# Kernel optimization log

Hardware: AMD Instinct MI355X
Metric: run time of the kernel (lower is better)

## Reference

```python
import jax, jax.numpy as jnp
import numpy as np

NEG = -9e15
N_NODES, IN_DIM, H1, H2, HEADS, DEC, N_EDGES, B_PAIRS = 4096, 512, 256, 128, 4, 512, 131072, 4096


def setup_inputs() -> dict:
    key = jax.random.key(0)
    ks = jax.random.split(key, 24)
    d = {}
    d["x_o"] = jax.random.normal(ks[0], (N_NODES, IN_DIM), jnp.float32)
    d["x_a"] = jax.random.normal(ks[1], (N_NODES, IN_DIM), jnp.float32)
    d["edge_index"] = jax.random.randint(ks[2], (2, N_EDGES), 0, N_NODES)
    d["idx"] = jax.random.randint(ks[3], (2, B_PAIRS), 0, N_NODES)
    # GAT layer 1 (in=IN_DIM, out=H1), per-head stacked params
    d["W1"] = jax.random.normal(ks[4], (HEADS, IN_DIM, H1)) * (IN_DIM ** -0.5)
    d["a1"] = jax.random.normal(ks[5], (HEADS, 2 * H1)) * 0.1
    d["lin1"] = jax.random.normal(ks[6], (HEADS * H1, H1)) * ((HEADS * H1) ** -0.5)
    d["res1"] = jax.random.normal(ks[7], (IN_DIM, H1)) * (IN_DIM ** -0.5)
    # GAT layer 2 (in=H1, out=H2)
    d["W2"] = jax.random.normal(ks[8], (HEADS, H1, H2)) * (H1 ** -0.5)
    d["a2"] = jax.random.normal(ks[9], (HEADS, 2 * H2)) * 0.1
    d["lin2"] = jax.random.normal(ks[10], (HEADS * H2, H2)) * ((HEADS * H2) ** -0.5)
    d["res2"] = jax.random.normal(ks[11], (H1, H2)) * (H1 ** -0.5)
    # heads
    d["mlp1_w"] = jax.random.normal(ks[12], (H2, H2)) * (H2 ** -0.5)
    d["mlp1_b"] = jnp.zeros((H2,))
    d["disc_w"] = jax.random.normal(ks[13], (H2, H2)) * (H2 ** -0.5)
    d["disc_b"] = jnp.zeros(())
    d["dec1_w"] = jax.random.normal(ks[14], (2 * H2, DEC)) * ((2 * H2) ** -0.5)
    d["dec1_b"] = jnp.zeros((DEC,))
    d["dec2_w"] = jax.random.normal(ks[15], (DEC, 1)) * (DEC ** -0.5)
    d["dec2_b"] = jnp.zeros((1,))
    d["adv_w"] = jax.random.normal(ks[16], (H2, H2)) * (H2 ** -0.5)
    d["adv_b"] = jnp.zeros((H2,))
    return d


def _gat_residual_layer(h, mask, W, a, lin, res):
    # W: [H, Fin, Fo], a: [H, 2*Fo]. e_ij = leakyrelu(Wh_i . a[:Fo] + Wh_j . a[Fo:])
    # (algebraically identical to the NxN all-pairs concat @ a in the torch code).
    def head(Wk, ak):
        Wh = h @ Wk                      # [N, Fo]
        Fo = Wk.shape[1]
        src = Wh @ ak[:Fo]               # [N]
        dst = Wh @ ak[Fo:]               # [N]
        e = jax.nn.leaky_relu(src[:, None] + dst[None, :], 0.2)  # [N, N]
        att = jax.nn.softmax(jnp.where(mask, e, NEG), axis=1)
        return jax.nn.elu(att @ Wh)      # [N, Fo]

    heads = jax.vmap(head)(W, a)         # [H, N, Fo]
    Hn, N, Fo = heads.shape
    concat = jnp.transpose(heads, (1, 0, 2)).reshape(N, Hn * Fo)
    mh = jax.nn.elu(concat @ lin)
    return jax.nn.relu(mh + h @ res)     # relu(relu(x)) == relu(x); dropout off in eval


def reference(x_o, x_a, W1, a1, lin1, res1, W2, a2, lin2, res2,
              mlp1_w, mlp1_b, disc_w, disc_b, dec1_w, dec1_b,
              dec2_w, dec2_b, adv_w, adv_b, edge_index, idx):
    N = x_o.shape[0]
    mask = jnp.zeros((N, N), jnp.bool_).at[edge_index[0], edge_index[1]].set(True)

    def encode(x):
        h = _gat_residual_layer(x, mask, W1, a1, lin1, res1)
        h = _gat_residual_layer(h, mask, W2, a2, lin2, res2)
        return h

    x2_o = encode(x_o)                   # [N, H2]
    x2_o_a = encode(x_a)

    h_os = jax.nn.sigmoid(x2_o.mean(0)) @ mlp1_w + mlp1_b      # [H2]
    h_os_a = jax.nn.sigmoid(x2_o_a.mean(0)) @ mlp1_w + mlp1_b

    def disc(c, h_pl, h_mi):  # Bilinear(h, c) with out=1
        sc1 = (h_pl @ disc_w) @ c + disc_b
        sc2 = (h_mi @ disc_w) @ c + disc_b
        return jnp.stack([sc1, sc2], axis=1)                    # [N, 2]

    ret_os = disc(h_os, x2_o, x2_o_a)
    ret_os_a = disc(h_os_a, x2_o_a, x2_o)

    # extract_entities, default branch (task_type not in {LDA, MDA, LMI})
    entity1 = x2_o[idx[0]]
    entity2 = x2_o[idx[1]]
    z = jnp.concatenate([entity1, entity2], axis=1)             # [B, 2*H2]
    hdec = jax.nn.relu(z @ dec1_w + dec1_b)
    log1 = hdec @ dec2_w + dec2_b                               # [B, 1]
    log = jax.nn.sigmoid(log1)

    sc_1 = (x2_o @ adv_w + adv_b).sum(1)[None, :]               # [1, N]
    sc_2 = (x2_o_a @ adv_w + adv_b).sum(1)[None, :]
    logits = jnp.concatenate([sc_1, sc_2], axis=1)              # [1, 2N]

    return (log, ret_os, ret_os_a, x2_o, logits, log1)
```

## Files before the change

kernel.cpp:

```cpp
#include <hip/hip_runtime.h>
#include <stdint.h>

#define N_NODES 4096
#define N_EDGES 131072

typedef __attribute__((ext_vector_type(8))) short short8;
typedef __attribute__((ext_vector_type(4))) float floatx4;

__device__ __forceinline__ float bf2f(unsigned short u) {
  union { unsigned u; float f; } v; v.u = ((unsigned)u) << 16; return v.f;
}
__device__ __forceinline__ unsigned short f2bf(float f) {
  union { float f; unsigned u; } v; v.f = f;
  unsigned r = 0x7FFFu + ((v.u >> 16) & 1u);
  return (unsigned short)((v.u + r) >> 16);
}
__device__ __forceinline__ float wredsum(float x) {
#pragma unroll
  for (int d = 32; d >= 1; d >>= 1) x += __shfl_xor(x, d);
  return x;
}
__device__ __forceinline__ float wredmax(float x) {
#pragma unroll
  for (int d = 32; d >= 1; d >>= 1) x = fmaxf(x, __shfl_xor(x, d));
  return x;
}
__device__ __forceinline__ void gload16(const void* g, void* l) {
  __builtin_amdgcn_global_load_lds(
      (const __attribute__((address_space(1))) unsigned*)g,
      (__attribute__((address_space(3))) unsigned*)l, 16, 0, 0);
}

__global__ __launch_bounds__(256) void gemm128(
    const unsigned short* __restrict__ A, const unsigned short* __restrict__ Bt,
    int M, int N, int K, unsigned short* __restrict__ Cb) {
  __shared__ __align__(16) unsigned short As[128 * 32];
  __shared__ __align__(16) unsigned short Bs[128 * 32];
  const int t = threadIdx.x, lane = t & 63, w = t >> 6;
  const int wr = w >> 1, wc = w & 1;
  const int n0 = blockIdx.x * 128, m0 = blockIdx.y * 128;
  floatx4 acc[4][4] = {};
  const int arow = t >> 2;
  const int schunk = (t & 3) ^ ((arow >> 1) & 3);

  for (int kt = 0; kt < K; kt += 32) {
    __syncthreads();
    gload16(A + (size_t)(m0 + arow) * K + kt + schunk * 8, &As[t * 8]);
    gload16(A + (size_t)(m0 + 64 + arow) * K + kt + schunk * 8, &As[(256 + t) * 8]);
    gload16(Bt + (size_t)(n0 + arow) * K + kt + schunk * 8, &Bs[t * 8]);
    gload16(Bt + (size_t)(n0 + 64 + arow) * K + kt + schunk * 8, &Bs[(256 + t) * 8]);
    __syncthreads();
    short8 af[4], bfr[4];
    const int koff = lane >> 4;
#pragma unroll
    for (int m = 0; m < 4; ++m) {
      const int r = wr * 64 + (lane & 15) + m * 16;
      af[m] = *(const short8*)&As[r * 32 + ((koff ^ ((r >> 1) & 3)) << 3)];
    }
#pragma unroll
    for (int n = 0; n < 4; ++n) {
      const int r = wc * 64 + (lane & 15) + n * 16;
      bfr[n] = *(const short8*)&Bs[r * 32 + ((koff ^ ((r >> 1) & 3)) << 3)];
    }
#pragma unroll
    for (int m = 0; m < 4; ++m)
#pragma unroll
      for (int n = 0; n < 4; ++n)
        acc[m][n] = __builtin_amdgcn_mfma_f32_16x16x32_bf16(af[m], bfr[n], acc[m][n], 0, 0, 0);
  }

  const int rb = m0 + wr * 64 + (lane >> 4) * 4;
  const int cb = n0 + wc * 64 + (lane & 15);
#pragma unroll
  for (int m = 0; m < 4; ++m)
#pragma unroll
    for (int n = 0; n < 4; ++n) {
      const int col = cb + n * 16;
#pragma unroll
      for (int r = 0; r < 4; ++r) {
        const int row = rb + m * 16 + r;
        Cb[(size_t)row * N + col] = f2bf(acc[m][n][r]);
      }
    }
}

__device__ __forceinline__ void stage64(const unsigned short* __restrict__ G,
                                        unsigned short* lds, int row0, int K,
                                        int kt, int t) {
  const int l0 = t, l1 = t + 256;
  const int r0 = l0 >> 3, c0 = l0 & 7;
  const int r1 = l1 >> 3, c1 = l1 & 7;
  gload16(G + (size_t)(row0 + r0) * K + kt + ((c0 ^ (r0 & 7)) << 3), &lds[l0 * 8]);
  gload16(G + (size_t)(row0 + r1) * K + kt + ((c1 ^ (r1 & 7)) << 3), &lds[l1 * 8]);
}
__device__ __forceinline__ short8 frag64(const unsigned short* lds, int r, int c) {
  return *(const short8*)&lds[r * 64 + ((c ^ (r & 7)) << 3)];
}

template <int EP>
__global__ __launch_bounds__(256) void gemm64(
    const unsigned short* __restrict__ A, const unsigned short* __restrict__ Bt,
    int M, int N, int K, unsigned short* __restrict__ Cb,
    const float* __restrict__ bias) {
  __shared__ __align__(16) unsigned short As[64 * 64];
  __shared__ __align__(16) unsigned short Bs[64 * 64];
  const int t = threadIdx.x, lane = t & 63, w = t >> 6;
  const int wr = w >> 1, wc = w & 1;
  const int n0 = blockIdx.x * 64, m0 = blockIdx.y * 64;
  floatx4 acc[2][2] = {};

  for (int kt = 0; kt < K; kt += 64) {
    __syncthreads();
    stage64(A, As, m0, K, kt, t);
    stage64(Bt, Bs, n0, K, kt, t);
    __syncthreads();
    short8 af[2][2], bfv[2][2];
#pragma unroll
    for (int m = 0; m < 2; ++m) {
      const int ra = wr * 32 + (lane & 15) + m * 16;
#pragma unroll
      for (int kk = 0; kk < 2; ++kk)
        af[m][kk] = frag64(As, ra, (lane >> 4) + kk * 4);
    }
#pragma unroll
    for (int n = 0; n < 2; ++n) {
      const int rb = wc * 32 + (lane & 15) + n * 16;
#pragma unroll
      for (int kk = 0; kk < 2; ++kk)
        bfv[n][kk] = frag64(Bs, rb, (lane >> 4) + kk * 4);
    }
#pragma unroll
    for (int kk = 0; kk < 2; ++kk)
#pragma unroll
      for (int m = 0; m < 2; ++m)
#pragma unroll
        for (int n = 0; n < 2; ++n)
          acc[m][n] = __builtin_amdgcn_mfma_f32_16x16x32_bf16(af[m][kk], bfv[n][kk], acc[m][n], 0, 0, 0);
  }

  const int rb = m0 + wr * 32 + (lane >> 4) * 4;
  const int cb = n0 + wc * 32 + (lane & 15);
#pragma unroll
  for (int m = 0; m < 2; ++m)
#pragma unroll
    for (int n = 0; n < 2; ++n) {
      const int col = cb + n * 16;
#pragma unroll
      for (int r = 0; r < 4; ++r) {
        const int row = rb + m * 16 + r;
        float v = acc[m][n][r];
        if (EP == 4) { v += bias[col]; v = v > 0.f ? v : 0.f; }
        Cb[(size_t)row * N + col] = f2bf(v);
      }
    }
}

template <int EP>
__global__ __launch_bounds__(256) void gemm64dual(
    const unsigned short* __restrict__ A1, const unsigned short* __restrict__ B1t, int K1,
    const unsigned short* __restrict__ A2, const unsigned short* __restrict__ B2t, int K2,
    int N, unsigned short* __restrict__ Cb,
    float* __restrict__ Cfo, float* __restrict__ Cfa) {
  __shared__ __align__(16) unsigned short As[64 * 64];
  __shared__ __align__(16) unsigned short Bs[64 * 64];
  const int t = threadIdx.x, lane = t & 63, w = t >> 6;
  const int wr = w >> 1, wc = w & 1;
  const int n0 = blockIdx.x * 64, m0 = blockIdx.y * 64;
  floatx4 acc[2][2] = {};

#pragma unroll 1
  for (int pass = 0; pass < 2; ++pass) {
    const unsigned short* A = pass ? A2 : A1;
    const unsigned short* Bt = pass ? B2t : B1t;
    const int K = pass ? K2 : K1;
    for (int kt = 0; kt < K; kt += 64) {
      __syncthreads();
      stage64(A, As, m0, K, kt, t);
      stage64(Bt, Bs, n0, K, kt, t);
      __syncthreads();
      short8 af[2][2], bfv[2][2];
#pragma unroll
      for (int m = 0; m < 2; ++m) {
        const int ra = wr * 32 + (lane & 15) + m * 16;
#pragma unroll
        for (int kk = 0; kk < 2; ++kk)
          af[m][kk] = frag64(As, ra, (lane >> 4) + kk * 4);
      }
#pragma unroll
      for (int n = 0; n < 2; ++n) {
        const int rb = wc * 32 + (lane & 15) + n * 16;
#pragma unroll
        for (int kk = 0; kk < 2; ++kk)
          bfv[n][kk] = frag64(Bs, rb, (lane >> 4) + kk * 4);
      }
#pragma unroll
      for (int kk = 0; kk < 2; ++kk)
#pragma unroll
        for (int m = 0; m < 2; ++m)
#pragma unroll
          for (int n = 0; n < 2; ++n)
            acc[m][n] = __builtin_amdgcn_mfma_f32_16x16x32_bf16(af[m][kk], bfv[n][kk], acc[m][n], 0, 0, 0);
    }
    if (pass == 0) {
#pragma unroll
      for (int m = 0; m < 2; ++m)
#pragma unroll
        for (int n = 0; n < 2; ++n)
#pragma unroll
          for (int r = 0; r < 4; ++r) {
            float v = acc[m][n][r];
            acc[m][n][r] = v > 0.f ? v : expm1f(v);
          }
    }
  }

  const int rb = m0 + wr * 32 + (lane >> 4) * 4;
  const int cb = n0 + wc * 32 + (lane & 15);
#pragma unroll
  for (int m = 0; m < 2; ++m)
#pragma unroll
    for (int n = 0; n < 2; ++n) {
      const int col = cb + n * 16;
#pragma unroll
      for (int r = 0; r < 4; ++r) {
        const int row = rb + m * 16 + r;
        float v = acc[m][n][r];
        v = v > 0.f ? v : 0.f;
        if (EP == 0) {
          Cb[(size_t)row * N + col] = f2bf(v);
        } else {
          float* bb = (row < 4096) ? Cfo : Cfa;
          bb[(size_t)(row & 4095) * N + col] = v;
        }
      }
    }
}

__global__ __launch_bounds__(256) void scatter_kernel(
    const int* __restrict__ ei, unsigned long long* __restrict__ mb) {
  int e = blockIdx.x * 256 + threadIdx.x;
  if (e < N_EDGES) {
    int r = ei[e], c = ei[N_EDGES + e];
    atomicOr(&mb[(size_t)r * 64 + (c >> 6)], 1ull << (c & 63));
  }
}

__global__ __launch_bounds__(256) void pack2_kernel(
    const float* W1, const float* lin1, const float* res1, const float* W2,
    const float* lin2, const float* res2, const float* dec1,
    const float* xo, const float* xa,
    unsigned short* dW1, unsigned short* dlin1, unsigned short* dres1,
    unsigned short* dW2, unsigned short* dlin2, unsigned short* dres2,
    unsigned short* ddec1, unsigned short* x16) {
  const int b = blockIdx.x, t = threadIdx.x;
  if (b >= 1248) {
    int ib = b - 1248;
    const float* src = (ib < 512) ? xo : xa;
    unsigned short* dst = x16 + ((ib < 512) ? 0 : (size_t)4096 * 512);
    size_t base = (size_t)(ib & 511) * 4096;
#pragma unroll
    for (int q = 0; q < 4; ++q) {
      size_t o = base + q * 1024 + t * 4;
      float4 v = *(const float4*)&src[o];
      ushort4 u = {f2bf(v.x), f2bf(v.y), f2bf(v.z), f2bf(v.w)};
      *(ushort4*)&dst[o] = u;
    }
    return;
  }
  const float* src; unsigned short* dst; int K, F, nFt, tb;
  if (b < 512)       { int h = b >> 7;        src = W1 + h * 131072; dst = dW1 + h * 131072; K = 512;  F = 256; nFt = 8;  tb = b & 127; }
  else if (b < 768)  {                        src = lin1;            dst = dlin1;            K = 1024; F = 256; nFt = 8;  tb = b - 512; }
  else if (b < 896)  {                        src = res1;            dst = dres1;            K = 512;  F = 256; nFt = 8;  tb = b - 768; }
  else if (b < 1024) { int h = (b - 896) >> 5; src = W2 + h * 32768; dst = dW2 + h * 32768;  K = 256;  F = 128; nFt = 4;  tb = (b - 896) & 31; }
  else if (b < 1088) {                        src = lin2;            dst = dlin2;            K = 512;  F = 128; nFt = 4;  tb = b - 1024; }
  else if (b < 1120) {                        src = res2;            dst = dres2;            K = 256;  F = 128; nFt = 4;  tb = b - 1088; }
  else               {                        src = dec1;            dst = ddec1;            K = 256;  F = 512; nFt = 16; tb = b - 1120; }
  const int k0 = (tb / nFt) * 32, f0 = (tb % nFt) * 32;
  __shared__ float tile[32][33];
  {
    int r = t >> 3, c4 = (t & 7) * 4;
    float4 v = *(const float4*)&src[(size_t)(k0 + r) * F + f0 + c4];
    tile[r][c4] = v.x; tile[r][c4 + 1] = v.y; tile[r][c4 + 2] = v.z; tile[r][c4 + 3] = v.w;
  }
  __syncthreads();
  {
    int f = t >> 3, k4 = (t & 7) * 4;
    ushort4 u;
    u.x = f2bf(tile[k4 + 0][f]); u.y = f2bf(tile[k4 + 1][f]);
    u.z = f2bf(tile[k4 + 2][f]); u.w = f2bf(tile[k4 + 3][f]);
    *(ushort4*)&dst[(size_t)(f0 + f) * K + k0 + k4] = u;
  }
}

__global__ __launch_bounds__(256) void srcdst_kernel(
    const unsigned short* __restrict__ Wh, const float* __restrict__ a,
    float* __restrict__ sd, int FO) {
  int lane = threadIdx.x & 63, wv = threadIdx.x >> 6;
  int i = blockIdx.x * 4 + wv;
  int W = 4 * FO;
  for (int h = 0; h < 4; ++h) {
    float s = 0.f, d = 0.f;
    for (int f = lane; f < FO; f += 64) {
      float wh = bf2f(Wh[(size_t)i * W + h * FO + f]);
      s += wh * a[h * 2 * FO + f];
      d += wh * a[h * 2 * FO + FO + f];
    }
    s = wredsum(s);
    d = wredsum(d);
    if (lane == 0) { sd[i * 8 + h] = s; sd[i * 8 + 4 + h] = d; }
  }
}

template <int FO>
__global__ __launch_bounds__(256) void attn_kernel(
    const unsigned long long* __restrict__ mb, const float* __restrict__ sd,
    const unsigned short* __restrict__ Wh, unsigned short* __restrict__ outp) {
  constexpr int E = FO / 64;
  constexpr int W = 4 * FO;
  constexpr int WGCAP = 512;
  __shared__ unsigned short nbr[4104];
  __shared__ float wgs[4][WGCAP + 8];
  __shared__ int s_cnt;
  const int i = blockIdx.x;
  const int mrow = i & 4095;
  const int base = i & ~4095;
  const int t = threadIdx.x;
  const int lane = t & 63, h = t >> 6;

  if (t < 64) {
    unsigned long long wb = mb[(size_t)mrow * 64 + t];
    int pc = __popcll(wb);
    int inc = pc;
#pragma unroll
    for (int d = 1; d < 64; d <<= 1) {
      int v = __shfl_up(inc, d);
      if (t >= d) inc += v;
    }
    if (t == 63) s_cnt = inc;
    int off = inc - pc;
    while (wb) {
      int b = __builtin_ctzll(wb);
      nbr[off++] = (unsigned short)(t * 64 + b);
      wb &= wb - 1;
    }
  }
  __syncthreads();
  const int cnt = s_cnt;
  if (t < 8) nbr[(cnt + t < 4103) ? cnt + t : 4103] = 0;
  const float src_i = sd[(size_t)i * 8 + h];
  float acc[E] = {};
  float inv = 1.f;
  if (cnt > 0) {
    float m = -1e30f;
    for (int nn = lane; nn < cnt; nn += 64) {
      int j = base + nbr[nn];
      float x = src_i + sd[(size_t)j * 8 + 4 + h];
      m = fmaxf(m, x > 0.f ? x : 0.2f * x);
    }
    m = wredmax(m);
    float ssum = 0.f;
    for (int nn = lane; nn < cnt; nn += 64) {
      int j = base + nbr[nn];
      float x = src_i + sd[(size_t)j * 8 + 4 + h];
      float e = x > 0.f ? x : 0.2f * x;
      float g = __expf(e - m);
      if (nn < WGCAP) wgs[h][nn] = g;
      ssum += g;
    }
    ssum = wredsum(ssum);
    inv = 1.f / ssum;
    if (lane < 8) wgs[h][((cnt < WGCAP ? cnt : WGCAP) + lane)] = 0.f;
    __builtin_amdgcn_s_barrier();
    const int lim = cnt < WGCAP ? cnt : WGCAP;
    const int limr = (lim + 7) & ~7;
    for (int nn = 0; nn < limr; nn += 8) {
      ushort4 ja = *(const ushort4*)&nbr[nn];
      ushort4 jb = *(const ushort4*)&nbr[nn + 4];
      float4 wa = *(const float4*)&wgs[h][nn];
      float4 wb4 = *(const float4*)&wgs[h][nn + 4];
      const int js[8] = {ja.x, ja.y, ja.z, ja.w, jb.x, jb.y, jb.z, jb.w};
      const float ws[8] = {wa.x, wa.y, wa.z, wa.w, wb4.x, wb4.y, wb4.z, wb4.w};
      if constexpr (E == 4) {
        uint2 r[8];
#pragma unroll
        for (int q = 0; q < 8; ++q)
          r[q] = *(const uint2*)(Wh + (size_t)(base + js[q]) * W + h * FO + lane * E);
#pragma unroll
        for (int q = 0; q < 8; ++q) {
          acc[0] += ws[q] * bf2f((unsigned short)(r[q].x & 0xffff));
          acc[1] += ws[q] * bf2f((unsigned short)(r[q].x >> 16));
          acc[2] += ws[q] * bf2f((unsigned short)(r[q].y & 0xffff));
          acc[3] += ws[q] * bf2f((unsigned short)(r[q].y >> 16));
        }
      } else {
        unsigned r[8];
#pragma unroll
        for (int q = 0; q < 8; ++q)
          r[q] = *(const unsigned*)(Wh + (size_t)(base + js[q]) * W + h * FO + lane * E);
#pragma unroll
        for (int q = 0; q < 8; ++q) {
          acc[0] += ws[q] * bf2f((unsigned short)(r[q] & 0xffff));
          acc[1] += ws[q] * bf2f((unsigned short)(r[q] >> 16));
        }
      }
    }
    for (int nn = WGCAP; nn < cnt; ++nn) {
      int j = base + nbr[nn];
      float x = src_i + sd[(size_t)j * 8 + 4 + h];
      float e = x > 0.f ? x : 0.2f * x;
      float g = __expf(e - m);
      const unsigned short* p = Wh + (size_t)j * W + h * FO + lane * E;
#pragma unroll
      for (int q = 0; q < E; ++q) acc[q] += g * bf2f(p[q]);
    }
  } else {
    const float wg = 1.f / 4096.f;
    for (int j = 0; j < N_NODES; ++j) {
      const unsigned short* p = Wh + (size_t)(base + j) * W + h * FO + lane * E;
#pragma unroll
      for (int q = 0; q < E; ++q) acc[q] += wg * bf2f(p[q]);
    }
  }
  unsigned short* op = outp + (size_t)i * W + h * FO + lane * E;
#pragma unroll
  for (int q = 0; q < E; ++q) {
    float v = acc[q] * inv;
    op[q] = f2bf(v > 0.f ? v : expm1f(v));
  }
}

__global__ __launch_bounds__(128) void colsum_kernel(
    const float* __restrict__ x2o, const float* __restrict__ x2a,
    float* __restrict__ small) {
  int b = blockIdx.x, f = threadIdx.x;
  const float* x = (b < 64) ? x2o : x2a;
  float* s = (b < 64) ? small : (small + 128);
  int r0 = (b & 63) * 64;
  float acc = 0.f;
  for (int r = 0; r < 64; ++r) acc += x[(size_t)(r0 + r) * 128 + f];
  atomicAdd(&s[f], acc);
}

__global__ __launch_bounds__(128) void finalize_kernel(
    float* __restrict__ small, const float* __restrict__ mlp1_w,
    const float* __restrict__ mlp1_b, const float* __restrict__ disc_w,
    const float* __restrict__ adv_w, const float* __restrict__ adv_b) {
  __shared__ float so[128], sa[128], ho[128], ha[128];
  int f = threadIdx.x;
  so[f] = 1.f / (1.f + __expf(-small[f] * (1.f / 4096.f)));
  sa[f] = 1.f / (1.f + __expf(-small[128 + f] * (1.f / 4096.f)));
  __syncthreads();
  float aco = mlp1_b[f], aca = mlp1_b[f];
  for (int c = 0; c < 128; ++c) {
    aco += so[c] * mlp1_w[c * 128 + f];
    aca += sa[c] * mlp1_w[c * 128 + f];
  }
  ho[f] = aco;
  ha[f] = aca;
  __syncthreads();
  float vo = 0.f, va = 0.f, ar = 0.f;
  for (int c = 0; c < 128; ++c) {
    vo += disc_w[f * 128 + c] * ho[c];
    va += disc_w[f * 128 + c] * ha[c];
    ar += adv_w[f * 128 + c];
  }
  small[256 + f] = vo;
  small[384 + f] = va;
  small[512 + f] = ar;
  if (f == 0) {
    float b = 0.f;
    for (int c = 0; c < 128; ++c) b += adv_b[c];
    small[640] = b;
  }
}

__global__ __launch_bounds__(256) void pernode_kernel(
    const float* __restrict__ x2o, const float* __restrict__ x2a,
    const float* __restrict__ small, const float* __restrict__ disc_b,
    float* __restrict__ out) {
  const float* v_os = small + 256;
  const float* v_a = small + 384;
  const float* adv_rs = small + 512;
  int lane = threadIdx.x & 63, wv = threadIdx.x >> 6;
  int i = blockIdx.x * 4 + wv;
  float2 xo = *(const float2*)&x2o[(size_t)i * 128 + lane * 2];
  float2 xa = *(const float2*)&x2a[(size_t)i * 128 + lane * 2];
  float2 vo = *(const float2*)&v_os[lane * 2];
  float2 va = *(const float2*)&v_a[lane * 2];
  float2 ar = *(const float2*)&adv_rs[lane * 2];
  float poo = wredsum(xo.x * vo.x + xo.y * vo.y);
  float pao = wredsum(xa.x * vo.x + xa.y * vo.y);
  float paa = wredsum(xa.x * va.x + xa.y * va.y);
  float poa = wredsum(xo.x * va.x + xo.y * va.y);
  float pov = wredsum(xo.x * ar.x + xo.y * ar.y);
  float pav = wredsum(xa.x * ar.x + xa.y * ar.y);
  if (lane == 0) {
    float db = disc_b[0], bv = small[640];
    out[4096 + 2 * i] = poo + db;
    out[4096 + 2 * i + 1] = pao + db;
    out[12288 + 2 * i] = paa + db;
    out[12288 + 2 * i + 1] = poa + db;
    out[544768 + i] = pov + bv;
    out[548864 + i] = pav + bv;
  }
}

__global__ __launch_bounds__(256) void gather_kernel(
    const float* __restrict__ x2o, const int* __restrict__ idx,
    unsigned short* __restrict__ z) {
  int i = blockIdx.x, c = threadIdx.x;
  int s = (c < 128) ? idx[i] : idx[4096 + i];
  z[(size_t)i * 256 + c] = f2bf(x2o[(size_t)s * 128 + (c & 127)]);
}

__global__ __launch_bounds__(256) void dec2_kernel(
    const unsigned short* __restrict__ hdec, const float* __restrict__ w2,
    const float* __restrict__ b2, float* __restrict__ out) {
  int lane = threadIdx.x & 63, wv = threadIdx.x >> 6;
  int i = blockIdx.x * 4 + wv;
  float s = 0.f;
#pragma unroll
  for (int q = 0; q < 8; ++q) {
    int f = lane + q * 64;
    s += bf2f(hdec[(size_t)i * 512 + f]) * w2[f];
  }
  s = wredsum(s);
  if (lane == 0) {
    float v = s + b2[0];
    out[552960 + i] = v;
    out[i] = 1.f / (1.f + __expf(-v));
  }
}

extern "C" void kernel_launch(void* const* d_in, const int* in_sizes, int n_in,
                              void* d_out, int out_size, void* d_ws, size_t ws_size,
                              hipStream_t stream) {
  const float* x_o = (const float*)d_in[0];
  const float* x_a = (const float*)d_in[1];
  const int* ei = (const int*)d_in[2];
  const int* idx = (const int*)d_in[3];
  const float* W1 = (const float*)d_in[4];
  const float* a1 = (const float*)d_in[5];
  const float* lin1 = (const float*)d_in[6];
  const float* res1 = (const float*)d_in[7];
  const float* W2 = (const float*)d_in[8];
  const float* a2 = (const float*)d_in[9];
  const float* lin2 = (const float*)d_in[10];
  const float* res2 = (const float*)d_in[11];
  const float* mlp1_w = (const float*)d_in[12];
  const float* mlp1_b = (const float*)d_in[13];
  const float* disc_w = (const float*)d_in[14];
  const float* disc_b = (const float*)d_in[15];
  const float* dec1_w = (const float*)d_in[16];
  const float* dec1_b = (const float*)d_in[17];
  const float* dec2_w = (const float*)d_in[18];
  const float* dec2_b = (const float*)d_in[19];
  const float* adv_w = (const float*)d_in[20];
  const float* adv_b = (const float*)d_in[21];
  float* out = (float*)d_out;

  char* w = (char*)d_ws;
  size_t off = 0;
  auto alloc = [&](size_t b) {
    char* p = w + off;
    off += (b + 255) & ~(size_t)255;
    return p;
  };
  unsigned long long* mb = (unsigned long long*)alloc((size_t)4096 * 64 * 8);
  unsigned short* x16 = (unsigned short*)alloc((size_t)8192 * 512 * 2);
  unsigned short* Wh1 = (unsigned short*)alloc((size_t)8192 * 1024 * 2);
  unsigned short* ho1 = (unsigned short*)alloc((size_t)8192 * 1024 * 2);
  unsigned short* h1 = (unsigned short*)alloc((size_t)8192 * 256 * 2);
  unsigned short* Wh2 = (unsigned short*)alloc((size_t)8192 * 512 * 2);
  unsigned short* ho2 = (unsigned short*)alloc((size_t)8192 * 512 * 2);
  float* x2a = (float*)alloc((size_t)4096 * 128 * 4);
  float* sd1 = (float*)alloc((size_t)8192 * 8 * 4);
  float* sd2 = (float*)alloc((size_t)8192 * 8 * 4);
  float* small = (float*)alloc(1024 * 4);
  unsigned short* tW1 = (unsigned short*)alloc((size_t)524288 * 2);
  unsigned short* tlin1 = (unsigned short*)alloc((size_t)262144 * 2);
  unsigned short* tres1 = (unsigned short*)alloc((size_t)131072 * 2);
  unsigned short* tW2 = (unsigned short*)alloc((size_t)131072 * 2);
  unsigned short* tlin2 = (unsigned short*)alloc((size_t)65536 * 2);
  unsigned short* tres2 = (unsigned short*)alloc((size_t)32768 * 2);
  unsigned short* tdec1 = (unsigned short*)alloc((size_t)131072 * 2);
  unsigned short* z16 = (unsigned short*)alloc((size_t)4096 * 256 * 2);
  unsigned short* hdec = (unsigned short*)alloc((size_t)4096 * 512 * 2);

  hipMemsetAsync(mb, 0, (size_t)4096 * 64 * 8, stream);
  hipMemsetAsync(small, 0, 1024, stream);
  scatter_kernel<<<512, 256, 0, stream>>>(ei, mb);
  pack2_kernel<<<2272, 256, 0, stream>>>(W1, lin1, res1, W2, lin2, res2, dec1_w,
                                         x_o, x_a, tW1, tlin1, tres1, tW2,
                                         tlin2, tres2, tdec1, x16);

  float* x2o_out = out + 20480;

  gemm128<<<dim3(8, 64), 256, 0, stream>>>(x16, tW1, 8192, 1024, 512, Wh1);
  srcdst_kernel<<<2048, 256, 0, stream>>>(Wh1, a1, sd1, 256);
  attn_kernel<256><<<8192, 256, 0, stream>>>(mb, sd1, Wh1, ho1);
  gemm64dual<0><<<dim3(4, 128), 256, 0, stream>>>(ho1, tlin1, 1024, x16, tres1, 512, 256, h1, nullptr, nullptr);
  gemm128<<<dim3(4, 64), 256, 0, stream>>>(h1, tW2, 8192, 512, 256, Wh2);
  srcdst_kernel<<<2048, 256, 0, stream>>>(Wh2, a2, sd2, 128);
  attn_kernel<128><<<8192, 256, 0, stream>>>(mb, sd2, Wh2, ho2);
  gemm64dual<1><<<dim3(2, 128), 256, 0, stream>>>(ho2, tlin2, 512, h1, tres2, 256, 128, nullptr, x2o_out, x2a);

  colsum_kernel<<<128, 128, 0, stream>>>(x2o_out, x2a, small);
  finalize_kernel<<<1, 128, 0, stream>>>(small, mlp1_w, mlp1_b, disc_w, adv_w, adv_b);
  pernode_kernel<<<1024, 256, 0, stream>>>(x2o_out, x2a, small, disc_b, out);
  gather_kernel<<<4096, 256, 0, stream>>>(x2o_out, idx, z16);
  gemm64<4><<<dim3(8, 64), 256, 0, stream>>>(z16, tdec1, 4096, 512, 256, hdec, dec1_b);
  dec2_kernel<<<1024, 256, 0, stream>>>(hdec, dec2_w, dec2_b, out);
}
```

Baseline: 215.5 us.

## Fuse src/dst attention scores into GEMM epilogue and split neighbors across waves

Removes the separate srcdst kernels. The per-node attention projections are now computed in the gemm128 epilogue, reduced with shuffles and accumulated with atomics into sd buffers that the scatter kernel zeros. The attention kernel now splits the neighbor list across all four waves, each wave covering every head, and sums the partial results through LDS. Nodes with no neighbors take an early-exit path. The aim is fewer launches and better load balance and locality in neighbor aggregation. The cost is extra atomics, more registers for the per-head accumulators, and an extra LDS reduction.

```diff
diff --git a/kernel.cpp b/kernel.cpp
--- a/kernel.cpp
+++ b/kernel.cpp
@@ -33,7 +33,8 @@
 
 __global__ __launch_bounds__(256) void gemm128(
     const unsigned short* __restrict__ A, const unsigned short* __restrict__ Bt,
-    int M, int N, int K, unsigned short* __restrict__ Cb) {
+    int M, int N, int K, unsigned short* __restrict__ Cb,
+    const float* __restrict__ avec, float* __restrict__ sdv, int FO) {
   __shared__ __align__(16) unsigned short As[128 * 32];
   __shared__ __align__(16) unsigned short Bs[128 * 32];
   const int t = threadIdx.x, lane = t & 63, w = t >> 6;
@@ -82,6 +83,38 @@
         Cb[(size_t)row * N + col] = f2bf(acc[m][n][r]);
       }
     }
+
+  if (avec) {
+    const int h = n0 / FO;
+    const int cw0 = cb - h * FO;
+    float as_[4], ad_[4];
+#pragma unroll
+    for (int n = 0; n < 4; ++n) {
+      as_[n] = avec[h * 2 * FO + cw0 + n * 16];
+      ad_[n] = avec[h * 2 * FO + FO + cw0 + n * 16];
+    }
+#pragma unroll
+    for (int m = 0; m < 4; ++m)
+#pragma unroll
+      for (int r = 0; r < 4; ++r) {
+        float sp = 0.f, dp = 0.f;
+#pragma unroll
+        for (int n = 0; n < 4; ++n) {
+          sp += acc[m][n][r] * as_[n];
+          dp += acc[m][n][r] * ad_[n];
+        }
+#pragma unroll
+        for (int d = 1; d < 16; d <<= 1) {
+          sp += __shfl_xor(sp, d);
+          dp += __shfl_xor(dp, d);
+        }
+        if ((lane & 15) == 0) {
+          const int row = rb + m * 16 + r;
+          atomicAdd(&sdv[row * 8 + h], sp);
+          atomicAdd(&sdv[row * 8 + 4 + h], dp);
+        }
+      }
+  }
 }
 
 __device__ __forceinline__ void stage64(const unsigned short* __restrict__ G,
@@ -237,11 +270,17 @@
 }
 
 __global__ __launch_bounds__(256) void scatter_kernel(
-    const int* __restrict__ ei, unsigned long long* __restrict__ mb) {
-  int e = blockIdx.x * 256 + threadIdx.x;
-  if (e < N_EDGES) {
+    const int* __restrict__ ei, unsigned long long* __restrict__ mb,
+    float* __restrict__ sd1, float* __restrict__ sd2) {
+  int b = blockIdx.x;
+  if (b < 512) {
+    int e = b * 256 + threadIdx.x;
     int r = ei[e], c = ei[N_EDGES + e];
     atomicOr(&mb[(size_t)r * 64 + (c >> 6)], 1ull << (c & 63));
+  } else {
+    int z = (b - 512) * 256 + threadIdx.x;
+    if (z < 65536) sd1[z] = 0.f;
+    else sd2[z - 65536] = 0.f;
   }
 }
 
@@ -292,25 +331,6 @@
   }
 }
 
-__global__ __launch_bounds__(256) void srcdst_kernel(
-    const unsigned short* __restrict__ Wh, const float* __restrict__ a,
-    float* __restrict__ sd, int FO) {
-  int lane = threadIdx.x & 63, wv = threadIdx.x >> 6;
-  int i = blockIdx.x * 4 + wv;
-  int W = 4 * FO;
-  for (int h = 0; h < 4; ++h) {
-    float s = 0.f, d = 0.f;
-    for (int f = lane; f < FO; f += 64) {
-      float wh = bf2f(Wh[(size_t)i * W + h * FO + f]);
-      s += wh * a[h * 2 * FO + f];
-      d += wh * a[h * 2 * FO + FO + f];
-    }
-    s = wredsum(s);
-    d = wredsum(d);
-    if (lane == 0) { sd[i * 8 + h] = s; sd[i * 8 + 4 + h] = d; }
-  }
-}
-
 template <int FO>
 __global__ __launch_bounds__(256) void attn_kernel(
     const unsigned long long* __restrict__ mb, const float* __restrict__ sd,
@@ -318,14 +338,17 @@
   constexpr int E = FO / 64;
   constexpr int W = 4 * FO;
   constexpr int WGCAP = 512;
-  __shared__ unsigned short nbr[4104];
-  __shared__ float wgs[4][WGCAP + 8];
+  __shared__ __align__(16) char smem[8208 + 8320];
+  unsigned short* nbr = (unsigned short*)smem;
+  float (*wgs)[520] = (float (*)[520])(smem + 8208);
+  float* red = (float*)smem;
   __shared__ int s_cnt;
+  __shared__ float s_inv[4];
   const int i = blockIdx.x;
   const int mrow = i & 4095;
   const int base = i & ~4095;
   const int t = threadIdx.x;
-  const int lane = t & 63, h = t >> 6;
+  const int lane = t & 63, wv = t >> 6;
 
   if (t < 64) {
     unsigned long long wb = mb[(size_t)mrow * 64 + t];
@@ -346,39 +369,59 @@
   }
   __syncthreads();
   const int cnt = s_cnt;
+
+  if (cnt == 0) {
+    const float wg = 1.f / 4096.f;
+    float acc0[E] = {};
+    for (int j = 0; j < N_NODES; ++j) {
+      const unsigned short* p = Wh + (size_t)(base + j) * W + wv * FO + lane * E;
+#pragma unroll
+      for (int q = 0; q < E; ++q) acc0[q] += wg * bf2f(p[q]);
+    }
+    unsigned short* op = outp + (size_t)i * W + wv * FO + lane * E;
+#pragma unroll
+    for (int q = 0; q < E; ++q) {
+      float v = acc0[q];
+      op[q] = f2bf(v > 0.f ? v : expm1f(v));
+    }
+    return;
+  }
+
   if (t < 8) nbr[(cnt + t < 4103) ? cnt + t : 4103] = 0;
-  const float src_i = sd[(size_t)i * 8 + h];
-  float acc[E] = {};
-  float inv = 1.f;
-  if (cnt > 0) {
-    float m = -1e30f;
-    for (int nn = lane; nn < cnt; nn += 64) {
-      int j = base + nbr[nn];
-      float x = src_i + sd[(size_t)j * 8 + 4 + h];
-      m = fmaxf(m, x > 0.f ? x : 0.2f * x);
-    }
-    m = wredmax(m);
-    float ssum = 0.f;
-    for (int nn = lane; nn < cnt; nn += 64) {
-      int j = base + nbr[nn];
-      float x = src_i + sd[(size_t)j * 8 + 4 + h];
-      float e = x > 0.f ? x : 0.2f * x;
-      float g = __expf(e - m);
-      if (nn < WGCAP) wgs[h][nn] = g;
-      ssum += g;
-    }
-    ssum = wredsum(ssum);
-    inv = 1.f / ssum;
-    if (lane < 8) wgs[h][((cnt < WGCAP ? cnt : WGCAP) + lane)] = 0.f;
-    __builtin_amdgcn_s_barrier();
-    const int lim = cnt < WGCAP ? cnt : WGCAP;
-    const int limr = (lim + 7) & ~7;
-    for (int nn = 0; nn < limr; nn += 8) {
-      ushort4 ja = *(const ushort4*)&nbr[nn];
-      ushort4 jb = *(const ushort4*)&nbr[nn + 4];
+  const float src_i = sd[(size_t)i * 8 + wv];
+  float m = -1e30f;
+  for (int nn = lane; nn < cnt; nn += 64) {
+    int j = base + nbr[nn];
+    float x = src_i + sd[(size_t)j * 8 + 4 + wv];
+    m = fmaxf(m, x > 0.f ? x : 0.2f * x);
+  }
+  m = wredmax(m);
+  float ssum = 0.f;
+  for (int nn = lane; nn < cnt; nn += 64) {
+    int j = base + nbr[nn];
+    float x = src_i + sd[(size_t)j * 8 + 4 + wv];
+    float e = x > 0.f ? x : 0.2f * x;
+    float g = __expf(e - m);
+    if (nn < WGCAP) wgs[wv][nn] = g;
+    ssum += g;
+  }
+  ssum = wredsum(ssum);
+  if (lane == 0) s_inv[wv] = 1.f / ssum;
+  if (lane < 8) wgs[wv][(cnt < WGCAP ? cnt : WGCAP) + lane] = 0.f;
+  __syncthreads();
+
+  float acc[4][E] = {};
+  const int lim = cnt < WGCAP ? cnt : WGCAP;
+  const int ngroups = (lim + 7) >> 3;
+  for (int g = wv; g < ngroups; g += 4) {
+    const int nn = g * 8;
+    ushort4 ja = *(const ushort4*)&nbr[nn];
+    ushort4 jb = *(const ushort4*)&nbr[nn + 4];
+    const int js[8] = {ja.x, ja.y, ja.z, ja.w, jb.x, jb.y, jb.z, jb.w};
+#pragma unroll
+    for (int h = 0; h < 4; ++h) {
       float4 wa = *(const float4*)&wgs[h][nn];
       float4 wb4 = *(const float4*)&wgs[h][nn + 4];
-      const int js[8] = {ja.x, ja.y, ja.z, ja.w, jb.x, jb.y, jb.z, jb.w};
       const float ws[8] = {wa.x, wa.y, wa.z, wa.w, wb4.x, wb4.y, wb4.z, wb4.w};
       if constexpr (E == 4) {
         uint2 r[8];
@@ -387,10 +430,10 @@
           r[q] = *(const uint2*)(Wh + (size_t)(base + js[q]) * W + h * FO + lane * E);
 #pragma unroll
         for (int q = 0; q < 8; ++q) {
-          acc[0] += ws[q] * bf2f((unsigned short)(r[q].x & 0xffff));
-          acc[1] += ws[q] * bf2f((unsigned short)(r[q].x >> 16));
-          acc[2] += ws[q] * bf2f((unsigned short)(r[q].y & 0xffff));
-          acc[3] += ws[q] * bf2f((unsigned short)(r[q].y >> 16));
+          acc[h][0] += ws[q] * bf2f((unsigned short)(r[q].x & 0xffff));
+          acc[h][1] += ws[q] * bf2f((unsigned short)(r[q].x >> 16));
+          acc[h][2] += ws[q] * bf2f((unsigned short)(r[q].y & 0xffff));
+          acc[h][3] += ws[q] * bf2f((unsigned short)(r[q].y >> 16));
         }
       } else {
         unsigned r[8];
@@ -399,32 +442,39 @@
           r[q] = *(const unsigned*)(Wh + (size_t)(base + js[q]) * W + h * FO + lane * E);
 #pragma unroll
         for (int q = 0; q < 8; ++q) {
-          acc[0] += ws[q] * bf2f((unsigned short)(r[q] & 0xffff));
-          acc[1] += ws[q] * bf2f((unsigned short)(r[q] >> 16));
+          acc[h][0] += ws[q] * bf2f((unsigned short)(r[q] & 0xffff));
+          acc[h][1] += ws[q] * bf2f((unsigned short)(r[q] >> 16));
         }
       }
     }
-    for (int nn = WGCAP; nn < cnt; ++nn) {
-      int j = base + nbr[nn];
-      float x = src_i + sd[(size_t)j * 8 + 4 + h];
-      float e = x > 0.f ? x : 0.2f * x;
-      float g = __expf(e - m);
-      const unsigned short* p = Wh + (size_t)j * W + h * FO + lane * E;
-#pragma unroll
-      for (int q = 0; q < E; ++q) acc[q] += g * bf2f(p[q]);
-    }
-  } else {
-    const float wg = 1.f / 4096.f;
-    for (int j = 0; j < N_NODES; ++j) {
-      const unsigned short* p = Wh + (size_t)(base + j) * W + h * FO + lane * E;
-#pragma unroll
-      for (int q = 0; q < E; ++q) acc[q] += wg * bf2f(p[q]);
-    }
-  }
-  unsigned short* op = outp + (size_t)i * W + h * FO + lane * E;
+  }
+  for (int nn = WGCAP; nn < cnt; ++nn) {
+    int j = base + nbr[nn];
+    float x = src_i + sd[(size_t)j * 8 + 4 + wv];
+    float e = x > 0.f ? x : 0.2f * x;
+    float g = __expf(e - m);
+    const unsigned short* p = Wh + (size_t)j * W + wv * FO + lane * E;
+#pragma unroll
+    for (int q = 0; q < E; ++q) acc[wv][q] += g * bf2f(p[q]);
+  }
+  __syncthreads();
+#pragma unroll
+  for (int h = 0; h < 4; ++h)
+#pragma unroll
+    for (int q = 0; q < E; ++q)
+      red[(wv * 4 + h) * 64 * E + lane * E + q] = acc[h][q];
+  __syncthreads();
+  float fin[E] = {};
+#pragma unroll
+  for (int w2 = 0; w2 < 4; ++w2)
+#pragma unroll
+    for (int q = 0; q < E; ++q)
+      fin[q] += red[(w2 * 4 + wv) * 64 * E + lane * E + q];
+  const float inv = s_inv[wv];
+  unsigned short* op = outp + (size_t)i * W + wv * FO + lane * E;
 #pragma unroll
   for (int q = 0; q < E; ++q) {
-    float v = acc[q] * inv;
+    float v = fin[q] * inv;
     op[q] = f2bf(v > 0.f ? v : expm1f(v));
   }
 }
@@ -589,19 +639,17 @@
 
   hipMemsetAsync(mb, 0, (size_t)4096 * 64 * 8, stream);
   hipMemsetAsync(small, 0, 1024, stream);
-  scatter_kernel<<<512, 256, 0, stream>>>(ei, mb);
+  scatter_kernel<<<1024, 256, 0, stream>>>(ei, mb, sd1, sd2);
   pack2_kernel<<<2272, 256, 0, stream>>>(W1, lin1, res1, W2, lin2, res2, dec1_w,
                                          x_o, x_a, tW1, tlin1, tres1, tW2,
                                          tlin2, tres2, tdec1, x16);
 
   float* x2o_out = out + 20480;
 
-  gemm128<<<dim3(8, 64), 256, 0, stream>>>(x16, tW1, 8192, 1024, 512, Wh1);
-  srcdst_kernel<<<2048, 256, 0, stream>>>(Wh1, a1, sd1, 256);
+  gemm128<<<dim3(8, 64), 256, 0, stream>>>(x16, tW1, 8192, 1024, 512, Wh1, a1, sd1, 256);
   attn_kernel<256><<<8192, 256, 0, stream>>>(mb, sd1, Wh1, ho1);
   gemm64dual<0><<<dim3(4, 128), 256, 0, stream>>>(ho1, tlin1, 1024, x16, tres1, 512, 256, h1, nullptr, nullptr);
-  gemm128<<<dim3(4, 64), 256, 0, stream>>>(h1, tW2, 8192, 512, 256, Wh2);
-  srcdst_kernel<<<2048, 256, 0, stream>>>(Wh2, a2, sd2, 128);
+  gemm128<<<dim3(4, 64), 256, 0, stream>>>(h1, tW2, 8192, 512, 256, Wh2, a2, sd2, 128);
   attn_kernel<128><<<8192, 256, 0, stream>>>(mb, sd2, Wh2, ho2);
   gemm64dual<1><<<dim3(2, 128), 256, 0, stream>>>(ho2, tlin2, 512, h1, tres2, 256, 128, nullptr, x2o_out, x2a);
 
```

After: 232.6 us. +7.9%, slower.

## Fuse attention src/dst projections into GEMM epilogue and double-buffer neighbor gathers

Applied to the files above, without the earlier changes.

The per-node src/dst attention scores are now computed in the gemm128 epilogue from the fp32 accumulators, using shuffle reductions and atomicAdd into sd buffers. The scatter kernel zeroes those buffers first. This removes two srcdst kernel launches and the re-read of Wh from memory. Separately, the attention kernel's neighbor aggregation loop is software-pipelined with two register buffers of 8 gathered rows, so loads for the next group are in flight during the FMAs of the current one. The padding of the shared arrays is enlarged to cover the prefetch overrun. The costs are float atomics, whose ordering is nondeterministic and shifts scores slightly because they come from unrounded accumulators, plus higher register pressure in attn.

```diff
diff --git a/kernel.cpp b/kernel.cpp
--- a/kernel.cpp
+++ b/kernel.cpp
@@ -33,7 +33,8 @@
 
 __global__ __launch_bounds__(256) void gemm128(
     const unsigned short* __restrict__ A, const unsigned short* __restrict__ Bt,
-    int M, int N, int K, unsigned short* __restrict__ Cb) {
+    int M, int N, int K, unsigned short* __restrict__ Cb,
+    const float* __restrict__ avec, float* __restrict__ sdv, int FO) {
   __shared__ __align__(16) unsigned short As[128 * 32];
   __shared__ __align__(16) unsigned short Bs[128 * 32];
   const int t = threadIdx.x, lane = t & 63, w = t >> 6;
@@ -82,6 +83,38 @@
         Cb[(size_t)row * N + col] = f2bf(acc[m][n][r]);
       }
     }
+
+  if (avec) {
+    const int h = n0 / FO;
+    const int cw0 = cb - h * FO;
+    float as_[4], ad_[4];
+#pragma unroll
+    for (int n = 0; n < 4; ++n) {
+      as_[n] = avec[h * 2 * FO + cw0 + n * 16];
+      ad_[n] = avec[h * 2 * FO + FO + cw0 + n * 16];
+    }
+#pragma unroll
+    for (int m = 0; m < 4; ++m)
+#pragma unroll
+      for (int r = 0; r < 4; ++r) {
+        float sp = 0.f, dp = 0.f;
+#pragma unroll
+        for (int n = 0; n < 4; ++n) {
+          sp += acc[m][n][r] * as_[n];
+          dp += acc[m][n][r] * ad_[n];
+        }
+#pragma unroll
+        for (int d = 1; d < 16; d <<= 1) {
+          sp += __shfl_xor(sp, d);
+          dp += __shfl_xor(dp, d);
+        }
+        if ((lane & 15) == 0) {
+          const int row = rb + m * 16 + r;
+          atomicAdd(&sdv[row * 8 + h], sp);
+          atomicAdd(&sdv[row * 8 + 4 + h], dp);
+        }
+      }
+  }
 }
 
 __device__ __forceinline__ void stage64(const unsigned short* __restrict__ G,
@@ -237,11 +270,17 @@
 }
 
 __global__ __launch_bounds__(256) void scatter_kernel(
-    const int* __restrict__ ei, unsigned long long* __restrict__ mb) {
-  int e = blockIdx.x * 256 + threadIdx.x;
-  if (e < N_EDGES) {
+    const int* __restrict__ ei, unsigned long long* __restrict__ mb,
+    float* __restrict__ sd1, float* __restrict__ sd2) {
+  int b = blockIdx.x;
+  if (b < 512) {
+    int e = b * 256 + threadIdx.x;
     int r = ei[e], c = ei[N_EDGES + e];
     atomicOr(&mb[(size_t)r * 64 + (c >> 6)], 1ull << (c & 63));
+  } else {
+    int z = (b - 512) * 256 + threadIdx.x;
+    if (z < 65536) sd1[z] = 0.f;
+    else sd2[z - 65536] = 0.f;
   }
 }
 
@@ -292,25 +331,6 @@
   }
 }
 
-__global__ __launch_bounds__(256) void srcdst_kernel(
-    const unsigned short* __restrict__ Wh, const float* __restrict__ a,
-    float* __restrict__ sd, int FO) {
-  int lane = threadIdx.x & 63, wv = threadIdx.x >> 6;
-  int i = blockIdx.x * 4 + wv;
-  int W = 4 * FO;
-  for (int h = 0; h < 4; ++h) {
-    float s = 0.f, d = 0.f;
-    for (int f = lane; f < FO; f += 64) {
-      float wh = bf2f(Wh[(size_t)i * W + h * FO + f]);
-      s += wh * a[h * 2 * FO + f];
-      d += wh * a[h * 2 * FO + FO + f];
-    }
-    s = wredsum(s);
-    d = wredsum(d);
-    if (lane == 0) { sd[i * 8 + h] = s; sd[i * 8 + 4 + h] = d; }
-  }
-}
-
 template <int FO>
 __global__ __launch_bounds__(256) void attn_kernel(
     const unsigned long long* __restrict__ mb, const float* __restrict__ sd,
@@ -318,8 +338,8 @@
   constexpr int E = FO / 64;
   constexpr int W = 4 * FO;
   constexpr int WGCAP = 512;
-  __shared__ unsigned short nbr[4104];
-  __shared__ float wgs[4][WGCAP + 8];
+  __shared__ unsigned short nbr[4136];
+  __shared__ float wgs[4][WGCAP + 32];
   __shared__ int s_cnt;
   const int i = blockIdx.x;
   const int mrow = i & 4095;
@@ -346,7 +366,7 @@
   }
   __syncthreads();
   const int cnt = s_cnt;
-  if (t < 8) nbr[(cnt + t < 4103) ? cnt + t : 4103] = 0;
+  if (t < 40) nbr[(cnt + t < 4135) ? cnt + t : 4135] = 0;
   const float src_i = sd[(size_t)i * 8 + h];
   float acc[E] = {};
   float inv = 1.f;
@@ -369,40 +389,89 @@
     }
     ssum = wredsum(ssum);
     inv = 1.f / ssum;
-    if (lane < 8) wgs[h][((cnt < WGCAP ? cnt : WGCAP) + lane)] = 0.f;
+    const int limc = cnt < WGCAP ? cnt : WGCAP;
+    if (lane < 32) wgs[h][limc + lane] = 0.f;
     __builtin_amdgcn_s_barrier();
-    const int lim = cnt < WGCAP ? cnt : WGCAP;
-    const int limr = (lim + 7) & ~7;
-    for (int nn = 0; nn < limr; nn += 8) {
-      ushort4 ja = *(const ushort4*)&nbr[nn];
-      ushort4 jb = *(const ushort4*)&nbr[nn + 4];
-      float4 wa = *(const float4*)&wgs[h][nn];
-      float4 wb4 = *(const float4*)&wgs[h][nn + 4];
-      const int js[8] = {ja.x, ja.y, ja.z, ja.w, jb.x, jb.y, jb.z, jb.w};
-      const float ws[8] = {wa.x, wa.y, wa.z, wa.w, wb4.x, wb4.y, wb4.z, wb4.w};
-      if constexpr (E == 4) {
-        uint2 r[8];
-#pragma unroll
-        for (int q = 0; q < 8; ++q)
-          r[q] = *(const uint2*)(Wh + (size_t)(base + js[q]) * W + h * FO + lane * E);
-#pragma unroll
-        for (int q = 0; q < 8; ++q) {
-          acc[0] += ws[q] * bf2f((unsigned short)(r[q].x & 0xffff));
-          acc[1] += ws[q] * bf2f((unsigned short)(r[q].x >> 16));
-          acc[2] += ws[q] * bf2f((unsigned short)(r[q].y & 0xffff));
-          acc[3] += ws[q] * bf2f((unsigned short)(r[q].y >> 16));
-        }
-      } else {
-        unsigned r[8];
-#pragma unroll
-        for (int q = 0; q < 8; ++q)
-          r[q] = *(const unsigned*)(Wh + (size_t)(base + js[q]) * W + h * FO + lane * E);
-#pragma unroll
-        for (int q = 0; q < 8; ++q) {
-          acc[0] += ws[q] * bf2f((unsigned short)(r[q] & 0xffff));
-          acc[1] += ws[q] * bf2f((unsigned short)(r[q] >> 16));
-        }
-      }
+    const int ngroups = (limc + 7) >> 3;
+    const int ngr = (ngroups + 1) & ~1;
+    if constexpr (E == 4) {
+      uint2 rA[8], rB[8];
+#define LD8x2(R, g)                                                         \
+  {                                                                          \
+    const int nn_ = (g) * 8;                                                 \
+    ushort4 ja_ = *(const ushort4*)&nbr[nn_];                                \
+    ushort4 jb_ = *(const ushort4*)&nbr[nn_ + 4];                            \
+    R[0] = *(const uint2*)(Wh + (size_t)(base + ja_.x) * W + h * FO + lane * 4); \
+    R[1] = *(const uint2*)(Wh + (size_t)(base + ja_.y) * W + h * FO + lane * 4); \
+    R[2] = *(const uint2*)(Wh + (size_t)(base + ja_.z) * W + h * FO + lane * 4); \
+    R[3] = *(const uint2*)(Wh + (size_t)(base + ja_.w) * W + h * FO + lane * 4); \
+    R[4] = *(const uint2*)(Wh + (size_t)(base + jb_.x) * W + h * FO + lane * 4); \
+    R[5] = *(const uint2*)(Wh + (size_t)(base + jb_.y) * W + h * FO + lane * 4); \
+    R[6] = *(const uint2*)(Wh + (size_t)(base + jb_.z) * W + h * FO + lane * 4); \
+    R[7] = *(const uint2*)(Wh + (size_t)(base + jb_.w) * W + h * FO + lane * 4); \
+  }
+#define FMA8x2(R, g)                                                         \
+  {                                                                          \
+    const int nn_ = (g) * 8;                                                 \
+    float4 wa_ = *(const float4*)&wgs[h][nn_];                               \
+    float4 wb_ = *(const float4*)&wgs[h][nn_ + 4];                           \
+    const float ws_[8] = {wa_.x, wa_.y, wa_.z, wa_.w,                        \
+                          wb_.x, wb_.y, wb_.z, wb_.w};                       \
+    _Pragma("unroll") for (int q = 0; q < 8; ++q) {                          \
+      acc[0] += ws_[q] * bf2f((unsigned short)(R[q].x & 0xffff));            \
+      acc[1] += ws_[q] * bf2f((unsigned short)(R[q].x >> 16));               \
+      acc[2] += ws_[q] * bf2f((unsigned short)(R[q].y & 0xffff));            \
+      acc[3] += ws_[q] * bf2f((unsigned short)(R[q].y >> 16));               \
+    }                                                                        \
+  }
+      LD8x2(rA, 0);
+      LD8x2(rB, 1);
+      for (int g = 0; g < ngr; g += 2) {
+        FMA8x2(rA, g);
+        LD8x2(rA, g + 2);
+        FMA8x2(rB, g + 1);
+        LD8x2(rB, g + 3);
+      }
+#undef LD8x2
+#undef FMA8x2
+    } else {
+      unsigned rA[8], rB[8];
+#define LD8x1(R, g)                                                          \
+  {                                                                          \
+    const int nn_ = (g) * 8;                                                 \
+    ushort4 ja_ = *(const ushort4*)&nbr[nn_];                                \
+    ushort4 jb_ = *(const ushort4*)&nbr[nn_ + 4];                            \
+    R[0] = *(const unsigned*)(Wh + (size_t)(base + ja_.x) * W + h * FO + lane * 2); \
+    R[1] = *(const unsigned*)(Wh + (size_t)(base + ja_.y) * W + h * FO + lane * 2); \
+    R[2] = *(const unsigned*)(Wh + (size_t)(base + ja_.z) * W + h * FO + lane * 2); \
+    R[3] = *(const unsigned*)(Wh + (size_t)(base + ja_.w) * W + h * FO + lane * 2); \
+    R[4] = *(const unsigned*)(Wh + (size_t)(base + jb_.x) * W + h * FO + lane * 2); \
+    R[5] = *(const unsigned*)(Wh + (size_t)(base + jb_.y) * W + h * FO + lane * 2); \
+    R[6] = *(const unsigned*)(Wh + (size_t)(base + jb_.z) * W + h * FO + lane * 2); \
+    R[7] = *(const unsigned*)(Wh + (size_t)(base + jb_.w) * W + h * FO + lane * 2); \
+  }
+#define FMA8x1(R, g)                                                         \
+  {                                                                          \
+    const int nn_ = (g) * 8;                                                 \
+    float4 wa_ = *(const float4*)&wgs[h][nn_];                               \
+    float4 wb_ = *(const float4*)&wgs[h][nn_ + 4];                           \
+    const float ws_[8] = {wa_.x, wa_.y, wa_.z, wa_.w,                        \
+                          wb_.x, wb_.y, wb_.z, wb_.w};                       \
+    _Pragma("unroll") for (int q = 0; q < 8; ++q) {                          \
+      acc[0] += ws_[q] * bf2f((unsigned short)(R[q] & 0xffff));              \
+      acc[1] += ws_[q] * bf2f((unsigned short)(R[q] >> 16));                 \
+    }                                                                        \
+  }
+      LD8x1(rA, 0);
+      LD8x1(rB, 1);
+      for (int g = 0; g < ngr; g += 2) {
+        FMA8x1(rA, g);
+        LD8x1(rA, g + 2);
+        FMA8x1(rB, g + 1);
+        LD8x1(rB, g + 3);
+      }
+#undef LD8x1
+#undef FMA8x1
     }
     for (int nn = WGCAP; nn < cnt; ++nn) {
       int j = base + nbr[nn];
@@ -589,19 +658,17 @@
 
   hipMemsetAsync(mb, 0, (size_t)4096 * 64 * 8, stream);
   hipMemsetAsync(small, 0, 1024, stream);
-  scatter_kernel<<<512, 256, 0, stream>>>(ei, mb);
+  scatter_kernel<<<1024, 256, 0, stream>>>(ei, mb, sd1, sd2);
   pack2_kernel<<<2272, 256, 0, stream>>>(W1, lin1, res1, W2, lin2, res2, dec1_w,
                                          x_o, x_a, tW1, tlin1, tres1, tW2,
                                          tlin2, tres2, tdec1, x16);
 
   float* x2o_out = out + 20480;
 
-  gemm128<<<dim3(8, 64), 256, 0, stream>>>(x16, tW1, 8192, 1024, 512, Wh1);
-  srcdst_kernel<<<2048, 256, 0, stream>>>(Wh1, a1, sd1, 256);
+  gemm128<<<dim3(8, 64), 256, 0, stream>>>(x16, tW1, 8192, 1024, 512, Wh1, a1, sd1, 256);
   attn_kernel<256><<<8192, 256, 0, stream>>>(mb, sd1, Wh1, ho1);
   gemm64dual<0><<<dim3(4, 128), 256, 0, stream>>>(ho1, tlin1, 1024, x16, tres1, 512, 256, h1, nullptr, nullptr);
-  gemm128<<<dim3(4, 64), 256, 0, stream>>>(h1, tW2, 8192, 512, 256, Wh2);
-  srcdst_kernel<<<2048, 256, 0, stream>>>(Wh2, a2, sd2, 128);
+  gemm128<<<dim3(4, 64), 256, 0, stream>>>(h1, tW2, 8192, 512, 256, Wh2, a2, sd2, 128);
   attn_kernel<128><<<8192, 256, 0, stream>>>(mb, sd2, Wh2, ho2);
   gemm64dual<1><<<dim3(2, 128), 256, 0, stream>>>(ho2, tlin2, 512, h1, tres2, 256, 128, nullptr, x2o_out, x2a);
 
```

Result: slower. 235.9 us (+9.5%).
